# Performance work log

Measured on AMD Instinct MI355X. Metric: run time of the kernel, lower is better.

Reference implementation:

```python
import jax, jax.numpy as jnp
import numpy as np

N = 1_000_000
HID = 128


def setup_inputs() -> dict:
    key = jax.random.key(0)
    ks = jax.random.split(key, 7)
    F = jax.random.normal(ks[0], (N, 2, 2), dtype=jnp.float32)
    # torch.nn.Linear init scale ~ 1/sqrt(fan_in); exact distribution irrelevant for a reference
    W1 = jax.random.normal(ks[1], (3, HID), dtype=jnp.float32) / np.sqrt(3.0)
    b1 = jax.random.normal(ks[2], (HID,), dtype=jnp.float32) * 0.01
    W2 = jax.random.normal(ks[3], (HID, HID), dtype=jnp.float32) / np.sqrt(HID)
    b2 = jax.random.normal(ks[4], (HID,), dtype=jnp.float32) * 0.01
    W3 = jax.random.normal(ks[5], (HID, 4), dtype=jnp.float32) / np.sqrt(HID)
    b3 = jax.random.normal(ks[6], (4,), dtype=jnp.float32) * 0.01
    return {"F": F, "W1": W1, "b1": b1, "W2": W2, "b2": b2, "W3": W3, "b3": b3}


def reference(F, W1, b1, W2, b2, W3, b3):
    # batched 2x2 SVD -> polar rotation R = U @ Vh
    U, sigma, Vh = jnp.linalg.svd(F)            # U,Vh: [N,2,2], sigma: [N,2]
    R = jnp.einsum('nij,njk->nik', U, Vh)       # [N,2,2]
    # invariants
    I1 = jnp.sum(sigma, axis=1) - 2.0                       # [N]
    I2 = jnp.einsum('nij,nij->n', F, F) - 1.0               # trace(F^T F) - 1
    I3 = jnp.linalg.det(F) - 1.0                            # [N]
    x = jnp.stack([I1, I2, I3], axis=1)                     # [N,3]
    # tiny MLP: 3 -> HID -> HID -> 4
    h = jax.nn.relu(x @ W1 + b1)
    h = jax.nn.relu(h @ W2 + b2)
    y = (h @ W3 + b3).reshape(-1, 2, 2)                     # [N,2,2]
    S = 0.5 * (y + jnp.swapaxes(y, 1, 2))                   # symmetrize
    P = jnp.einsum('nij,njk->nik', R, S)
    cauchy = jnp.einsum('nij,nkj->nik', P, F)               # P @ F^T
    return cauchy
```

## Files before the change

### kernel.cpp

```cpp
#include <hip/hip_runtime.h>
#include <hip/hip_bf16.h>
#include <math.h>

#define HID   128
#define TPB   256
#define TROWS 128
#define NBLK  768

typedef __attribute__((ext_vector_type(8))) short        short8v;
typedef __attribute__((ext_vector_type(4))) float        f32x4;
typedef __attribute__((ext_vector_type(4))) unsigned int uint4v;

#define MFMA(a, b, c) __builtin_amdgcn_mfma_f32_16x16x32_bf16((a), (b), (c), 0, 0, 0)
#define SCHED_FENCE() __builtin_amdgcn_sched_barrier(0)
#define BC8(x) __builtin_bit_cast(short8v, x)

__device__ __forceinline__ unsigned int pk2bf(float lo, float hi) {
    unsigned int r;
    asm("v_cvt_pk_bf16_f32 %0, %1, %2" : "=v"(r) : "v"(lo), "v"(hi));
    return r;
}
__device__ __forceinline__ float bfhi(float x) {
    unsigned int r;
    asm("v_cvt_pk_bf16_f32 %0, %1, %2" : "=v"(r) : "v"(0.f), "v"(x));
    return __builtin_bit_cast(float, r);
}
__device__ __forceinline__ f32x4 relu4(f32x4 v) {
    f32x4 r;
    r.x = fmaxf(v.x, 0.f); r.y = fmaxf(v.y, 0.f);
    r.z = fmaxf(v.z, 0.f); r.w = fmaxf(v.w, 0.f);
    return r;
}

__global__ __launch_bounds__(TPB, 2)
void stress_kernel(const float* __restrict__ F,
                   const float* __restrict__ W1, const float* __restrict__ b1,
                   const float* __restrict__ W2, const float* __restrict__ b2,
                   const float* __restrict__ W3, const float* __restrict__ b3,
                   float* __restrict__ out, int N)
{
    __shared__ uint4v sA2[2048];
    __shared__ uint4v sA1[512];
    __shared__ uint4v sA3[256];
    __shared__ f32x4  sY[TROWS];
    __shared__ __align__(16) float sb2[HID];

    const int tid  = threadIdx.x;
    const int lane = tid & 63;
    const int wid  = tid >> 6;
    const int g    = lane >> 4;
    const int lr   = lane & 15;

    for (int e = tid; e < 2048; e += TPB) {
        int l = e & 63, ks = (e >> 6) & 3, jt = e >> 8;
        int gg = l >> 4;
        int j  = (l & 15) + 16 * jt;
        #define K2(B) (4 * gg + ((B) & 3) + 16 * (2 * ks + ((B) >> 2)))
        uint4v v;
        v.x = pk2bf(W2[K2(0) * HID + j], W2[K2(1) * HID + j]);
        v.y = pk2bf(W2[K2(2) * HID + j], W2[K2(3) * HID + j]);
        v.z = pk2bf(W2[K2(4) * HID + j], W2[K2(5) * HID + j]);
        v.w = pk2bf(W2[K2(6) * HID + j], W2[K2(7) * HID + j]);
        #undef K2
        sA2[e] = v;
    }
    for (int e = tid; e < 512; e += TPB) {
        int l = e & 63, jt = e >> 6;
        int gg = l >> 4;
        int j  = (l & 15) + 16 * jt;
        float av[8];
        #pragma unroll
        for (int b = 0; b < 8; ++b) {
            int c = 8 * gg + b;
            float v;
            if      (c < 3)   v = W1[c * HID + j];
            else if (c < 6)   v = W1[(c - 3) * HID + j] - bfhi(W1[(c - 3) * HID + j]);
            else if (c < 9)   v = W1[(c - 6) * HID + j];
            else if (c == 9)  v = b1[j];
            else if (c == 10) v = b1[j] - bfhi(b1[j]);
            else              v = 0.f;
            av[b] = v;
        }
        uint4v v;
        v.x = pk2bf(av[0], av[1]); v.y = pk2bf(av[2], av[3]);
        v.z = pk2bf(av[4], av[5]); v.w = pk2bf(av[6], av[7]);
        sA1[e] = v;
    }
    for (int e = tid; e < 256; e += TPB) {
        int l = e & 63, ks2 = e >> 6;
        int gg = l >> 4, t = l & 15;
        float w[8];
        #pragma unroll
        for (int b = 0; b < 8; ++b) {
            int j = 4 * gg + (b & 3) + 16 * (2 * ks2 + (b >> 2));
            w[b] = (t < 4) ? W3[j * 4 + t] : 0.f;
        }
        uint4v v;
        v.x = pk2bf(w[0], w[1]); v.y = pk2bf(w[2], w[3]);
        v.z = pk2bf(w[4], w[5]); v.w = pk2bf(w[6], w[7]);
        sA3[e] = v;
    }
    for (int i = tid; i < HID; i += TPB) sb2[i] = b2[i];
    __syncthreads();

    const f32x4* pB2 = (const f32x4*)sb2;
    const f32x4  z4  = {0.f, 0.f, 0.f, 0.f};

    f32x4 b3v = z4;
    if (g == 0) b3v = *(const f32x4*)b3;

    const int nTiles = (N + TROWS - 1) / TROWS;
    const int tile0  = blockIdx.x;

    f32x4 fv = z4;
    {
        const int n = tile0 * TROWS + wid * 32 + lane;
        if (lane < 32 && tile0 < nTiles && n < N) fv = ((const f32x4*)F)[n];
    }

    for (int tile = tile0; tile < nTiles; tile += gridDim.x) {
        const int nbase = tile * TROWS + wid * 32;

        const float fa = fv.x, fb = fv.y, fc = fv.z, fd = fv.w;
        float x0, x1, x2, R00, R01, R10, R11;
        {
            const float J   = fa * fd - fb * fc;
            const float ss  = fa * fa + fb * fb + fc * fc + fd * fd;
            const float sgn = (J >= 0.f) ? 1.f : -1.f;
            const float s   = fmaxf(ss + 2.f * fabsf(J), 1e-30f);
            float inv;
            asm("v_rsq_f32 %0, %1" : "=v"(inv) : "v"(s));
            const float r = s * inv;
            x0 = r - 2.f; x1 = ss - 1.f; x2 = J - 1.f;
            R00 = (fa + sgn * fd) * inv; R01 = (fb - sgn * fc) * inv;
            R10 = (fc - sgn * fb) * inv; R11 = (fd + sgn * fa) * inv;
        }

        const f32x4 ba0 = pB2[g +  0], bb0 = pB2[g +  4];
        const f32x4 ba1 = pB2[g +  8], bb1 = pB2[g + 12];
        const f32x4 ba2 = pB2[g + 16], bb2 = pB2[g + 20];
        const f32x4 ba3 = pB2[g + 24], bb3 = pB2[g + 28];
        short8v a1P_0 = BC8(sA1[0 * 64 + lane]), a1P_1 = BC8(sA1[1 * 64 + lane]);
        short8v a1Q_0 = BC8(sA1[2 * 64 + lane]), a1Q_1 = BC8(sA1[3 * 64 + lane]);
        short8v a3f_0, a3f_1, a3f_2, a3f_3;

        short8v b1f_0, b1f_1;
        #define B1BUILD(RT, DST) {                                                 \
            const float bx0 = __shfl(x0, (RT) * 16 + lr, 64);                      \
            const float bx1 = __shfl(x1, (RT) * 16 + lr, 64);                      \
            const float bx2 = __shfl(x2, (RT) * 16 + lr, 64);                      \
            const float xl0 = bx0 - bfhi(bx0);                                     \
            const float xl1 = bx1 - bfhi(bx1);                                     \
            const float xl2 = bx2 - bfhi(bx2);                                     \
            uint4v u;                                                              \
            u.x = (g == 0) ? pk2bf(bx0, bx1) : ((g == 1) ? pk2bf(xl2, 1.f) : 0u);  \
            u.y = (g == 0) ? pk2bf(bx2, bx0) : ((g == 1) ? pk2bf(1.f, 0.f) : 0u);  \
            u.z = (g == 0) ? pk2bf(bx1, bx2) : 0u;                                 \
            u.w = (g == 0) ? pk2bf(xl0, xl1) : 0u;                                 \
            DST = __builtin_bit_cast(short8v, u);                                  \
        }
        B1BUILD(0, b1f_0) B1BUILD(1, b1f_1)
        #undef B1BUILD

        #define L1CALC(A0, A1, D00, D01, D10, D11)   \
            D00 = MFMA(A0, b1f_0, z4); D01 = MFMA(A0, b1f_1, z4); \
            D10 = MFMA(A1, b1f_0, z4); D11 = MFMA(A1, b1f_1, z4);
        f32x4 p00, p01, p10, p11, q00, q01, q10, q11;
        L1CALC(a1P_0, a1P_1, p00, p01, p10, p11)
        SCHED_FENCE();

        f32x4 acc_0_0 = ba0, acc_0_1 = ba0, acc_1_0 = bb0, acc_1_1 = bb0,
              acc_2_0 = ba1, acc_2_1 = ba1, acc_3_0 = bb1, acc_3_1 = bb1,
              acc_4_0 = ba2, acc_4_1 = ba2, acc_5_0 = bb2, acc_5_1 = bb2,
              acc_6_0 = ba3, acc_6_1 = ba3, acc_7_0 = bb3, acc_7_1 = bb3;

        short8v bf_0, bf_1;
        #define PACK2(H00, H01, H10, H11) {                                       \
            const f32x4 ra = relu4(H00), rb = relu4(H10);                         \
            const f32x4 rc = relu4(H01), rd = relu4(H11);                         \
            uint4v u0, u1;                                                        \
            u0.x = pk2bf(ra.x, ra.y); u0.y = pk2bf(ra.z, ra.w);                   \
            u0.z = pk2bf(rb.x, rb.y); u0.w = pk2bf(rb.z, rb.w);                   \
            u1.x = pk2bf(rc.x, rc.y); u1.y = pk2bf(rc.z, rc.w);                   \
            u1.z = pk2bf(rd.x, rd.y); u1.w = pk2bf(rd.z, rd.w);                   \
            bf_0 = BC8(u0); bf_1 = BC8(u1);                                       \
        }
        #define STEP(JT, RT) acc_##JT##_##RT = MFMA(af_##JT, bf_##RT, acc_##JT##_##RT)
        #define KSBLOCK(KS, H00, H01, H10, H11, NEXTPART) {                       \
            const short8v af_0 = BC8(sA2[(0*4+(KS))*64+lane]);                    \
            const short8v af_1 = BC8(sA2[(1*4+(KS))*64+lane]);                    \
            const short8v af_2 = BC8(sA2[(2*4+(KS))*64+lane]);                    \
            const short8v af_3 = BC8(sA2[(3*4+(KS))*64+lane]);                    \
            const short8v af_4 = BC8(sA2[(4*4+(KS))*64+lane]);                    \
            const short8v af_5 = BC8(sA2[(5*4+(KS))*64+lane]);                    \
            const short8v af_6 = BC8(sA2[(6*4+(KS))*64+lane]);                    \
            const short8v af_7 = BC8(sA2[(7*4+(KS))*64+lane]);                    \
            PACK2(H00, H01, H10, H11);                                            \
            NEXTPART;                                                             \
            __builtin_amdgcn_s_setprio(1);                                        \
            STEP(0,0); STEP(0,1); STEP(1,0); STEP(1,1);                           \
            STEP(2,0); STEP(2,1); STEP(3,0); STEP(3,1);                           \
            STEP(4,0); STEP(4,1); STEP(5,0); STEP(5,1);                           \
            STEP(6,0); STEP(6,1); STEP(7,0); STEP(7,1);                           \
            __builtin_amdgcn_s_setprio(0);                                        \
            SCHED_FENCE();                                                        \
        }

        KSBLOCK(0, p00, p01, p10, p11,
                a1P_0 = BC8(sA1[4 * 64 + lane]); a1P_1 = BC8(sA1[5 * 64 + lane]);
                L1CALC(a1Q_0, a1Q_1, q00, q01, q10, q11))

        {
            const int tn = tile + gridDim.x;
            const int nn = tn * TROWS + wid * 32 + lane;
            fv = z4;
            if (lane < 32 && tn < nTiles && nn < N) fv = ((const f32x4*)F)[nn];
        }

        KSBLOCK(1, q00, q01, q10, q11,
                a1Q_0 = BC8(sA1[6 * 64 + lane]); a1Q_1 = BC8(sA1[7 * 64 + lane]);
                L1CALC(a1P_0, a1P_1, p00, p01, p10, p11))
        KSBLOCK(2, p00, p01, p10, p11,
                a3f_0 = BC8(sA3[0 * 64 + lane]); a3f_1 = BC8(sA3[1 * 64 + lane]);
                a3f_2 = BC8(sA3[2 * 64 + lane]); a3f_3 = BC8(sA3[3 * 64 + lane]);
                L1CALC(a1Q_0, a1Q_1, q00, q01, q10, q11))
        KSBLOCK(3, q00, q01, q10, q11, )
        #undef KSBLOCK
        #undef STEP
        #undef PACK2
        #undef L1CALC

        f32x4 accY_0 = b3v, accY_1 = b3v;
        {
            #define L3K(KS2, JA, JB) {                                                \
                const f32x4 ha0 = relu4(acc_##JA##_0);                                \
                const f32x4 hb0 = relu4(acc_##JB##_0);                                \
                const f32x4 ha1 = relu4(acc_##JA##_1);                                \
                const f32x4 hb1 = relu4(acc_##JB##_1);                                \
                uint4v u0, u1;                                                        \
                u0.x = pk2bf(ha0.x, ha0.y); u0.y = pk2bf(ha0.z, ha0.w);               \
                u0.z = pk2bf(hb0.x, hb0.y); u0.w = pk2bf(hb0.z, hb0.w);               \
                u1.x = pk2bf(ha1.x, ha1.y); u1.y = pk2bf(ha1.z, ha1.w);               \
                u1.z = pk2bf(hb1.x, hb1.y); u1.w = pk2bf(hb1.z, hb1.w);               \
                accY_0 = MFMA(a3f_##KS2, BC8(u0), accY_0);                            \
                accY_1 = MFMA(a3f_##KS2, BC8(u1), accY_1);                            \
            }
            L3K(0, 0, 1) L3K(1, 2, 3) L3K(2, 4, 5) L3K(3, 6, 7)
            #undef L3K
        }
        SCHED_FENCE();

        if (lane < 16) {
            sY[wid * 32 +  0 + lr] = accY_0;
            sY[wid * 32 + 16 + lr] = accY_1;
        }
        {
            const f32x4 yv = sY[wid * 32 + (lane & 31)];
            const int nn = nbase + lane;
            if (lane < 32 && nn < N) {
                const float y0 = yv.x, y1 = yv.y, y2 = yv.z, y3 = yv.w;
                const float s01 = 0.5f * (y1 + y2);
                const float P00 = R00 * y0  + R01 * s01;
                const float P01 = R00 * s01 + R01 * y3;
                const float P10 = R10 * y0  + R11 * s01;
                const float P11 = R10 * s01 + R11 * y3;
                f32x4 o;
                o.x = P00 * fa + P01 * fb;
                o.y = P00 * fc + P01 * fd;
                o.z = P10 * fa + P11 * fb;
                o.w = P10 * fc + P11 * fd;
                ((f32x4*)out)[nn] = o;
            }
        }
        SCHED_FENCE();
    }
}

extern "C" void kernel_launch(void* const* d_in, const int* in_sizes, int n_in,
                              void* d_out, int out_size, void* d_ws, size_t ws_size,
                              hipStream_t stream) {
    const float* F  = (const float*)d_in[0];
    const float* W1 = (const float*)d_in[1];
    const float* b1 = (const float*)d_in[2];
    const float* W2 = (const float*)d_in[3];
    const float* b2 = (const float*)d_in[4];
    const float* W3 = (const float*)d_in[5];
    const float* b3 = (const float*)d_in[6];
    float* out = (float*)d_out;
    const int N = in_sizes[0] / 4;

    const int nTiles = (N + TROWS - 1) / TROWS;
    int grid = nTiles < NBLK ? nTiles : NBLK;
    stress_kernel<<<dim3(grid), dim3(TPB), 0, stream>>>(F, W1, b1, W2, b2, W3, b3, out, N);
}
```

Baseline: 52.25 us.

## Process 64 rows per wave with four row-tiles and packed bf16 relu

Each wave now handles 64 rows instead of 32, with four 16-row tiles, so every layer-2 A-fragment loaded from LDS feeds 32 MFMAs instead of 16 and all 64 lanes do the per-row SVD and epilogue work. Layer-1 MFMAs are now computed inside each k-slice block and interleaved with the layer-2 MFMAs. ReLU is applied after bf16 packing with a packed signed 16-bit max. The tile size and grid size change to match. The larger accumulator set (128 floats) raises register pressure and may spill or lower occupancy under launch bounds of 2 waves per SIMD.

```diff
diff --git a/kernel.cpp b/kernel.cpp
--- a/kernel.cpp
+++ b/kernel.cpp
@@ -4,8 +4,8 @@
 
 #define HID   128
 #define TPB   256
-#define TROWS 128
-#define NBLK  768
+#define TROWS 256
+#define NBLK  512
 
 typedef __attribute__((ext_vector_type(8))) short        short8v;
 typedef __attribute__((ext_vector_type(4))) float        f32x4;
@@ -25,10 +25,9 @@
     asm("v_cvt_pk_bf16_f32 %0, %1, %2" : "=v"(r) : "v"(0.f), "v"(x));
     return __builtin_bit_cast(float, r);
 }
-__device__ __forceinline__ f32x4 relu4(f32x4 v) {
-    f32x4 r;
-    r.x = fmaxf(v.x, 0.f); r.y = fmaxf(v.y, 0.f);
-    r.z = fmaxf(v.z, 0.f); r.w = fmaxf(v.w, 0.f);
+__device__ __forceinline__ unsigned int pkrelu(unsigned int x) {
+    unsigned int r;
+    asm("v_pk_max_i16 %0, %1, %2" : "=v"(r) : "v"(x), "v"(0u));
     return r;
 }
 
@@ -114,12 +113,12 @@
 
     f32x4 fv = z4;
     {
-        const int n = tile0 * TROWS + wid * 32 + lane;
-        if (lane < 32 && tile0 < nTiles && n < N) fv = ((const f32x4*)F)[n];
+        const int n = tile0 * TROWS + wid * 64 + lane;
+        if (tile0 < nTiles && n < N) fv = ((const f32x4*)F)[n];
     }
 
     for (int tile = tile0; tile < nTiles; tile += gridDim.x) {
-        const int nbase = tile * TROWS + wid * 32;
+        const int nbase = tile * TROWS + wid * 64;
 
         const float fa = fv.x, fb = fv.y, fc = fv.z, fd = fv.w;
         float x0, x1, x2, R00, R01, R10, R11;
@@ -136,15 +135,7 @@
             R10 = (fc - sgn * fb) * inv; R11 = (fd + sgn * fa) * inv;
         }
 
-        const f32x4 ba0 = pB2[g +  0], bb0 = pB2[g +  4];
-        const f32x4 ba1 = pB2[g +  8], bb1 = pB2[g + 12];
-        const f32x4 ba2 = pB2[g + 16], bb2 = pB2[g + 20];
-        const f32x4 ba3 = pB2[g + 24], bb3 = pB2[g + 28];
-        short8v a1P_0 = BC8(sA1[0 * 64 + lane]), a1P_1 = BC8(sA1[1 * 64 + lane]);
-        short8v a1Q_0 = BC8(sA1[2 * 64 + lane]), a1Q_1 = BC8(sA1[3 * 64 + lane]);
-        short8v a3f_0, a3f_1, a3f_2, a3f_3;
-
-        short8v b1f_0, b1f_1;
+        short8v b1f_0, b1f_1, b1f_2, b1f_3;
         #define B1BUILD(RT, DST) {                                                 \
             const float bx0 = __shfl(x0, (RT) * 16 + lr, 64);                      \
             const float bx1 = __shfl(x1, (RT) * 16 + lr, 64);                      \
@@ -159,34 +150,43 @@
             u.w = (g == 0) ? pk2bf(xl0, xl1) : 0u;                                 \
             DST = __builtin_bit_cast(short8v, u);                                  \
         }
-        B1BUILD(0, b1f_0) B1BUILD(1, b1f_1)
+        B1BUILD(0, b1f_0) B1BUILD(1, b1f_1) B1BUILD(2, b1f_2) B1BUILD(3, b1f_3)
         #undef B1BUILD
-
-        #define L1CALC(A0, A1, D00, D01, D10, D11)   \
-            D00 = MFMA(A0, b1f_0, z4); D01 = MFMA(A0, b1f_1, z4); \
-            D10 = MFMA(A1, b1f_0, z4); D11 = MFMA(A1, b1f_1, z4);
-        f32x4 p00, p01, p10, p11, q00, q01, q10, q11;
-        L1CALC(a1P_0, a1P_1, p00, p01, p10, p11)
         SCHED_FENCE();
 
-        f32x4 acc_0_0 = ba0, acc_0_1 = ba0, acc_1_0 = bb0, acc_1_1 = bb0,
-              acc_2_0 = ba1, acc_2_1 = ba1, acc_3_0 = bb1, acc_3_1 = bb1,
-              acc_4_0 = ba2, acc_4_1 = ba2, acc_5_0 = bb2, acc_5_1 = bb2,
-              acc_6_0 = ba3, acc_6_1 = ba3, acc_7_0 = bb3, acc_7_1 = bb3;
-
-        short8v bf_0, bf_1;
-        #define PACK2(H00, H01, H10, H11) {                                       \
-            const f32x4 ra = relu4(H00), rb = relu4(H10);                         \
-            const f32x4 rc = relu4(H01), rd = relu4(H11);                         \
-            uint4v u0, u1;                                                        \
-            u0.x = pk2bf(ra.x, ra.y); u0.y = pk2bf(ra.z, ra.w);                   \
-            u0.z = pk2bf(rb.x, rb.y); u0.w = pk2bf(rb.z, rb.w);                   \
-            u1.x = pk2bf(rc.x, rc.y); u1.y = pk2bf(rc.z, rc.w);                   \
-            u1.z = pk2bf(rd.x, rd.y); u1.w = pk2bf(rd.z, rd.w);                   \
-            bf_0 = BC8(u0); bf_1 = BC8(u1);                                       \
-        }
-        #define STEP(JT, RT) acc_##JT##_##RT = MFMA(af_##JT, bf_##RT, acc_##JT##_##RT)
-        #define KSBLOCK(KS, H00, H01, H10, H11, NEXTPART) {                       \
+        const f32x4 ba0 = pB2[g +  0], bb0 = pB2[g +  4];
+        const f32x4 ba1 = pB2[g +  8], bb1 = pB2[g + 12];
+        const f32x4 ba2 = pB2[g + 16], bb2 = pB2[g + 20];
+        const f32x4 ba3 = pB2[g + 24], bb3 = pB2[g + 28];
+        f32x4 acc_0_0 = ba0, acc_0_1 = ba0, acc_0_2 = ba0, acc_0_3 = ba0;
+        f32x4 acc_1_0 = bb0, acc_1_1 = bb0, acc_1_2 = bb0, acc_1_3 = bb0;
+        f32x4 acc_2_0 = ba1, acc_2_1 = ba1, acc_2_2 = ba1, acc_2_3 = ba1;
+        f32x4 acc_3_0 = bb1, acc_3_1 = bb1, acc_3_2 = bb1, acc_3_3 = bb1;
+        f32x4 acc_4_0 = ba2, acc_4_1 = ba2, acc_4_2 = ba2, acc_4_3 = ba2;
+        f32x4 acc_5_0 = bb2, acc_5_1 = bb2, acc_5_2 = bb2, acc_5_3 = bb2;
+        f32x4 acc_6_0 = ba3, acc_6_1 = ba3, acc_6_2 = ba3, acc_6_3 = ba3;
+        f32x4 acc_7_0 = bb3, acc_7_1 = bb3, acc_7_2 = bb3, acc_7_3 = bb3;
+        SCHED_FENCE();
+
+        #define PACK1(PA, PB, BF) {                                               \
+            uint4v u;                                                             \
+            u.x = pkrelu(pk2bf(PA.x, PA.y)); u.y = pkrelu(pk2bf(PA.z, PA.w));     \
+            u.z = pkrelu(pk2bf(PB.x, PB.y)); u.w = pkrelu(pk2bf(PB.z, PB.w));     \
+            BF = BC8(u);                                                          \
+        }
+        #define STEP8(RT, BF)                                                     \
+            acc_0_##RT = MFMA(af_0, BF, acc_0_##RT);                              \
+            acc_1_##RT = MFMA(af_1, BF, acc_1_##RT);                              \
+            acc_2_##RT = MFMA(af_2, BF, acc_2_##RT);                              \
+            acc_3_##RT = MFMA(af_3, BF, acc_3_##RT);                              \
+            acc_4_##RT = MFMA(af_4, BF, acc_4_##RT);                              \
+            acc_5_##RT = MFMA(af_5, BF, acc_5_##RT);                              \
+            acc_6_##RT = MFMA(af_6, BF, acc_6_##RT);                              \
+            acc_7_##RT = MFMA(af_7, BF, acc_7_##RT);
+
+        #define KSBLOCK(KS) {                                                     \
+            const short8v a1_0 = BC8(sA1[(2*(KS)  )*64+lane]);                    \
+            const short8v a1_1 = BC8(sA1[(2*(KS)+1)*64+lane]);                    \
             const short8v af_0 = BC8(sA2[(0*4+(KS))*64+lane]);                    \
             const short8v af_1 = BC8(sA2[(1*4+(KS))*64+lane]);                    \
             const short8v af_2 = BC8(sA2[(2*4+(KS))*64+lane]);                    \
@@ -195,69 +195,84 @@
             const short8v af_5 = BC8(sA2[(5*4+(KS))*64+lane]);                    \
             const short8v af_6 = BC8(sA2[(6*4+(KS))*64+lane]);                    \
             const short8v af_7 = BC8(sA2[(7*4+(KS))*64+lane]);                    \
-            PACK2(H00, H01, H10, H11);                                            \
-            NEXTPART;                                                             \
-            __builtin_amdgcn_s_setprio(1);                                        \
-            STEP(0,0); STEP(0,1); STEP(1,0); STEP(1,1);                           \
-            STEP(2,0); STEP(2,1); STEP(3,0); STEP(3,1);                           \
-            STEP(4,0); STEP(4,1); STEP(5,0); STEP(5,1);                           \
-            STEP(6,0); STEP(6,1); STEP(7,0); STEP(7,1);                           \
-            __builtin_amdgcn_s_setprio(0);                                        \
-            SCHED_FENCE();                                                        \
-        }
-
-        KSBLOCK(0, p00, p01, p10, p11,
-                a1P_0 = BC8(sA1[4 * 64 + lane]); a1P_1 = BC8(sA1[5 * 64 + lane]);
-                L1CALC(a1Q_0, a1Q_1, q00, q01, q10, q11))
-
+            f32x4 pA0, pB0, pA1, pB1, pA2, pB2_, pA3, pB3;                        \
+            pA0 = MFMA(a1_0, b1f_0, z4); pB0 = MFMA(a1_1, b1f_0, z4);             \
+            pA1 = MFMA(a1_0, b1f_1, z4); pB1 = MFMA(a1_1, b1f_1, z4);             \
+            SCHED_FENCE();                                                        \
+            {                                                                     \
+                short8v bf;                                                       \
+                PACK1(pA0, pB0, bf);                                              \
+                pA2 = MFMA(a1_0, b1f_2, z4); pB2_ = MFMA(a1_1, b1f_2, z4);        \
+                __builtin_amdgcn_s_setprio(1); STEP8(0, bf)                       \
+                __builtin_amdgcn_s_setprio(0);                                    \
+            }                                                                     \
+            SCHED_FENCE();                                                        \
+            {                                                                     \
+                short8v bf;                                                       \
+                PACK1(pA1, pB1, bf);                                              \
+                pA3 = MFMA(a1_0, b1f_3, z4); pB3 = MFMA(a1_1, b1f_3, z4);         \
+                __builtin_amdgcn_s_setprio(1); STEP8(1, bf)                       \
+                __builtin_amdgcn_s_setprio(0);                                    \
+            }                                                                     \
+            SCHED_FENCE();                                                        \
+            {                                                                     \
+                short8v bf;                                                       \
+                PACK1(pA2, pB2_, bf);                                             \
+                __builtin_amdgcn_s_setprio(1); STEP8(2, bf)                       \
+                __builtin_amdgcn_s_setprio(0);                                    \
+            }                                                                     \
+            SCHED_FENCE();                                                        \
+            {                                                                     \
+                short8v bf;                                                       \
+                PACK1(pA3, pB3, bf);                                              \
+                __builtin_amdgcn_s_setprio(1); STEP8(3, bf)                       \
+                __builtin_amdgcn_s_setprio(0);                                    \
+            }                                                                     \
+            SCHED_FENCE();                                                        \
+        }
+
+        KSBLOCK(0)
         {
             const int tn = tile + gridDim.x;
-            const int nn = tn * TROWS + wid * 32 + lane;
+            const int nn = tn * TROWS + wid * 64 + lane;
             fv = z4;
-            if (lane < 32 && tn < nTiles && nn < N) fv = ((const f32x4*)F)[nn];
-        }
-
-        KSBLOCK(1, q00, q01, q10, q11,
-                a1Q_0 = BC8(sA1[6 * 64 + lane]); a1Q_1 = BC8(sA1[7 * 64 + lane]);
-                L1CALC(a1P_0, a1P_1, p00, p01, p10, p11))
-        KSBLOCK(2, p00, p01, p10, p11,
-                a3f_0 = BC8(sA3[0 * 64 + lane]); a3f_1 = BC8(sA3[1 * 64 + lane]);
-                a3f_2 = BC8(sA3[2 * 64 + lane]); a3f_3 = BC8(sA3[3 * 64 + lane]);
-                L1CALC(a1Q_0, a1Q_1, q00, q01, q10, q11))
-        KSBLOCK(3, q00, q01, q10, q11, )
+            if (tn < nTiles && nn < N) fv = ((const f32x4*)F)[nn];
+        }
+        KSBLOCK(1)
+        KSBLOCK(2)
+        KSBLOCK(3)
         #undef KSBLOCK
-        #undef STEP
-        #undef PACK2
-        #undef L1CALC
-
-        f32x4 accY_0 = b3v, accY_1 = b3v;
+        #undef STEP8
+
+        f32x4 accY_0 = b3v, accY_1 = b3v, accY_2 = b3v, accY_3 = b3v;
+        #define L3RT(RT, JA, JB, A3) {                                            \
+            uint4v u;                                                             \
+            u.x = pkrelu(pk2bf(acc_##JA##_##RT.x, acc_##JA##_##RT.y));            \
+            u.y = pkrelu(pk2bf(acc_##JA##_##RT.z, acc_##JA##_##RT.w));            \
+            u.z = pkrelu(pk2bf(acc_##JB##_##RT.x, acc_##JB##_##RT.y));            \
+            u.w = pkrelu(pk2bf(acc_##JB##_##RT.z, acc_##JB##_##RT.w));            \
+            accY_##RT = MFMA(A3, BC8(u), accY_##RT);                              \
+        }
+        #define L3K(KS2, JA, JB) {                                                \
+            const short8v a3f = BC8(sA3[(KS2) * 64 + lane]);                      \
+            L3RT(0, JA, JB, a3f) L3RT(1, JA, JB, a3f)                             \
+            L3RT(2, JA, JB, a3f) L3RT(3, JA, JB, a3f)                             \
+        } SCHED_FENCE();
+        L3K(0, 0, 1) L3K(1, 2, 3) L3K(2, 4, 5) L3K(3, 6, 7)
+        #undef L3K
+        #undef L3RT
+        #undef PACK1
+
+        if (lane < 16) {
+            sY[wid * 64 +  0 + lr] = accY_0;
+            sY[wid * 64 + 16 + lr] = accY_1;
+            sY[wid * 64 + 32 + lr] = accY_2;
+            sY[wid * 64 + 48 + lr] = accY_3;
+        }
         {
-            #define L3K(KS2, JA, JB) {                                                \
-                const f32x4 ha0 = relu4(acc_##JA##_0);                                \
-                const f32x4 hb0 = relu4(acc_##JB##_0);                                \
-                const f32x4 ha1 = relu4(acc_##JA##_1);                                \
-                const f32x4 hb1 = relu4(acc_##JB##_1);                                \
-                uint4v u0, u1;                                                        \
-                u0.x = pk2bf(ha0.x, ha0.y); u0.y = pk2bf(ha0.z, ha0.w);               \
-                u0.z = pk2bf(hb0.x, hb0.y); u0.w = pk2bf(hb0.z, hb0.w);               \
-                u1.x = pk2bf(ha1.x, ha1.y); u1.y = pk2bf(ha1.z, ha1.w);               \
-                u1.z = pk2bf(hb1.x, hb1.y); u1.w = pk2bf(hb1.z, hb1.w);               \
-                accY_0 = MFMA(a3f_##KS2, BC8(u0), accY_0);                            \
-                accY_1 = MFMA(a3f_##KS2, BC8(u1), accY_1);                            \
-            }
-            L3K(0, 0, 1) L3K(1, 2, 3) L3K(2, 4, 5) L3K(3, 6, 7)
-            #undef L3K
-        }
-        SCHED_FENCE();
-
-        if (lane < 16) {
-            sY[wid * 32 +  0 + lr] = accY_0;
-            sY[wid * 32 + 16 + lr] = accY_1;
-        }
-        {
-            const f32x4 yv = sY[wid * 32 + (lane & 31)];
+            const f32x4 yv = sY[wid * 64 + lane];
             const int nn = nbase + lane;
-            if (lane < 32 && nn < N) {
+            if (nn < N) {
                 const float y0 = yv.x, y1 = yv.y, y2 = yv.z, y3 = yv.w;
                 const float s01 = 0.5f * (y1 + y2);
                 const float P00 = R00 * y0  + R01 * s01;
```

Measured after the change: 44.62 us, median of 2. -14.6%, faster.
